# Kernel tuning notes

Hardware: AMD Instinct MI355X
Metric: run time of the kernel (lower is better)

Reference implementation:

```python
import jax, jax.numpy as jnp
import numpy as np
from jax import lax

DIM = 1024
HEADS = 16
HEAD_DIM = DIM // HEADS
BLOCK = 128          # block_size_q == block_size_kv
DECAY = 0.9          # decay_factor
SPIKE_TH = 0.5       # spike_threshold
K_WINNERS = 4        # k-winner-take-all along head_dim
HIDDEN = 4 * DIM     # SwiGLU hidden_mult=4.0
EPS = 1e-5


def _rmsnorm(x, w):
    norm = lax.rsqrt(jnp.mean(x * x, axis=-1, keepdims=True) + EPS)
    return w * x * norm


def _spike_kwta(k):
    # spiking threshold: pass activation only above SPIKE_TH
    k = jnp.where(k > SPIKE_TH, k, 0.0)
    # k-winners-take-all along head_dim
    thr = lax.top_k(k, K_WINNERS)[0][..., -1:]  # [B,T,H,1]
    return jnp.where(k >= thr, k, 0.0)


def _mix(h, Wr, Wk, Wv, Wo):
    # chunkwise (blockwise) decayed linear attention, RWKV-style
    B, T, _ = h.shape
    N = T // BLOCK
    r = jax.nn.sigmoid((h @ Wr).reshape(B, T, HEADS, HEAD_DIM))  # receptance
    k = _spike_kwta((h @ Wk).reshape(B, T, HEADS, HEAD_DIM))
    v = (h @ Wv).reshape(B, T, HEADS, HEAD_DIM)

    def chunks(a):  # [B,T,H,D] -> [N,B,L,H,D]
        return a.reshape(B, N, BLOCK, HEADS, HEAD_DIM).transpose(1, 0, 2, 3, 4)

    rc_all, kc_all, vc_all = chunks(r), chunks(k), chunks(v)

    t_idx = jnp.arange(BLOCK, dtype=h.dtype)
    w_in = (DECAY ** (t_idx + 1.0))[None, :, None, None]        # weight on incoming state
    w_out = (DECAY ** (BLOCK - 1.0 - t_idx))[None, :, None, None]  # weight into next state
    lm = t_idx[:, None] - t_idx[None, :]
    mask = jnp.where(lm >= 0, DECAY ** lm, 0.0)                 # [L,L] causal decay
    w_L = DECAY ** BLOCK

    def step(S, inp):
        rc, kc, vc = inp  # each [B,L,H,D]
        inter = jnp.einsum('blhd,bhde->blhe', rc * w_in, S)
        A = jnp.einsum('blhd,bmhd->bhlm', rc, kc) * mask
        intra = jnp.einsum('bhlm,bmhe->blhe', A, vc)
        S_new = w_L * S + jnp.einsum('blhd,blhe->bhde', kc * w_out, vc)
        return S_new, inter + intra

    S0 = jnp.zeros((B, HEADS, HEAD_DIM, HEAD_DIM), h.dtype)
    _, y = lax.scan(step, S0, (rc_all, kc_all, vc_all))  # y: [N,B,L,H,D]
    y = y.transpose(1, 0, 2, 3, 4).reshape(B, T, DIM)
    return y @ Wo


def setup_inputs() -> dict:
    key = jax.random.key(0)
    ks = jax.random.split(key, 9)
    s = 0.02
    return {
        'x': jax.random.normal(ks[0], (2, 1024, DIM), jnp.float32),
        'norm1_w': jnp.ones((DIM,), jnp.float32),
        'Wr': jax.random.normal(ks[1], (DIM, DIM), jnp.float32) * s,
        'Wk': jax.random.normal(ks[2], (DIM, DIM), jnp.float32) * s + 0.5,
        'Wv': jax.random.normal(ks[3], (DIM, DIM), jnp.float32) * s,
        'Wo': jax.random.normal(ks[4], (DIM, DIM), jnp.float32) * s,
        'norm2_w': jnp.ones((DIM,), jnp.float32),
        'w1': jax.random.normal(ks[5], (DIM, HIDDEN), jnp.float32) * s,
        'w2': jax.random.normal(ks[6], (DIM, HIDDEN), jnp.float32) * s,
        'w3': jax.random.normal(ks[7], (HIDDEN, DIM), jnp.float32) * s,
    }


def reference(x, norm1_w, Wr, Wk, Wv, Wo, norm2_w, w1, w2, w3):
    x = x + _mix(_rmsnorm(x, norm1_w), Wr, Wk, Wv, Wo)
    h = _rmsnorm(x, norm2_w)
    x = x + (jax.nn.silu(h @ w1) * (h @ w2)) @ w3
    return x
```

## Files before the change

### kernel.cpp

```cpp
#include <hip/hip_runtime.h>
#include <hip/hip_bf16.h>
#include <math.h>


#define DIMD 1024
#define BT   2048
#define HEADS 16
#define HD   64
#define CHUNK 128
#define NCHUNK 8
#define HIDDEN 4096
#define WL_128 1.3900845e-06f
#define LOG2D  (-0.15200309344504997f)

typedef __attribute__((ext_vector_type(4))) float f32x4;
typedef __attribute__((ext_vector_type(8))) short bf16x8;

__device__ __forceinline__ unsigned short f2bf(float f) {
    __hip_bfloat16 h = __float2bfloat16(f);
    return __builtin_bit_cast(unsigned short, h);
}
__device__ __forceinline__ float bf2f(unsigned short u) {
    __hip_bfloat16 h = __builtin_bit_cast(__hip_bfloat16, u);
    return __bfloat162float(h);
}
__device__ __forceinline__ void gload_lds16(const void* g, void* l) {
    __builtin_amdgcn_global_load_lds(
        (const __attribute__((address_space(1))) void*)g,
        (__attribute__((address_space(3))) void*)l,
        16, 0, 0);
}

__global__ __launch_bounds__(256) void prep_kernel(const float* __restrict__ x,
                                                   const float* __restrict__ norm1w,
                                                   const float* __restrict__ Wr,
                                                   const float* __restrict__ Wv,
                                                   const float* __restrict__ Wo,
                                                   const float* __restrict__ Wk,
                                                   const float* __restrict__ w1,
                                                   const float* __restrict__ w2,
                                                   const float* __restrict__ w3,
                                                   unsigned short* __restrict__ BtA,
                                                   unsigned short* __restrict__ wo_t,
                                                   unsigned short* __restrict__ wkB,
                                                   unsigned short* __restrict__ w1t,
                                                   unsigned short* __restrict__ w2t,
                                                   unsigned short* __restrict__ w3t,
                                                   unsigned short* __restrict__ hI) {
    __shared__ float t[64][65];
    __shared__ float red[4];
    int bid = blockIdx.x;
    if (bid < 4096) {
        const float* src; unsigned short* dst; int K, N, tile, mode = 0;
        if (bid < 256)       { src = Wr; dst = BtA;                 K = 1024; N = 1024; tile = bid; }
        else if (bid < 512)  { src = Wv; dst = BtA + 1024 * 1024;   K = 1024; N = 1024; tile = bid - 256; }
        else if (bid < 768)  { src = Wo; dst = wo_t;                K = 1024; N = 1024; tile = bid - 512; }
        else if (bid < 1024) { src = Wk; dst = wkB;                 K = 1024; N = 1024; tile = bid - 768; mode = 1; }
        else if (bid < 2048) { src = w1; dst = w1t; K = 1024; N = 4096; tile = bid - 1024; }
        else if (bid < 3072) { src = w2; dst = w2t; K = 1024; N = 4096; tile = bid - 2048; }
        else                 { src = w3; dst = w3t; K = 4096; N = 1024; tile = bid - 3072; }
        int xt = N >> 6;
        int bn = (tile % xt) << 6, bk = (tile / xt) << 6;
        int tx = threadIdx.x & 15, ty = threadIdx.x >> 4;
        #pragma unroll
// ... 37 lines not shown
        const float* xr = x + (size_t)row * DIMD;
        int i0 = threadIdx.x * 4;
        float4 v = *reinterpret_cast<const float4*>(xr + i0);
        float ss = v.x*v.x + v.y*v.y + v.z*v.z + v.w*v.w;
        #pragma unroll
        for (int off = 32; off; off >>= 1) ss += __shfl_xor(ss, off);
        if ((threadIdx.x & 63) == 0) red[threadIdx.x >> 6] = ss;
        __syncthreads();
        ss = red[0] + red[1] + red[2] + red[3];
        float norm = rsqrtf(ss * (1.0f / DIMD) + 1e-5f);
        float4 wv = *reinterpret_cast<const float4*>(norm1w + i0);
        float o[4];
        o[0] = wv.x * v.x * norm; o[1] = wv.y * v.y * norm;
        o[2] = wv.z * v.z * norm; o[3] = wv.w * v.w * norm;
        ushort4 u0, u1;
        unsigned short* q0 = (unsigned short*)&u0;
        unsigned short* q1 = (unsigned short*)&u1;
        #pragma unroll
        for (int j = 0; j < 4; ++j) {
            q0[j] = f2bf(o[j]);
            q1[j] = f2bf(o[j] - bf2f(q0[j]));
        }
        *reinterpret_cast<ushort4*>(hI + (size_t)row * 2048 + i0) = u0;
        *reinterpret_cast<ushort4*>(hI + (size_t)row * 2048 + 1024 + i0) = u1;
    }
}

__global__ __launch_bounds__(256) void proj_kernel(const unsigned short* __restrict__ hI,
                                                   const unsigned short* __restrict__ BtA,
                                                   const unsigned short* __restrict__ wkB,
                                                   unsigned short* __restrict__ r16,
                                                   unsigned short* __restrict__ v16,
                                                   unsigned short* __restrict__ k16) {
    __shared__ __align__(16) short As[128 * 64];
    __shared__ __align__(16) short Bs[128 * 64];
    const int tid = threadIdx.x;
    const int wv = tid >> 6, ln = tid & 63;
    const int g = ln >> 4, r = ln & 15;
    const int srow_off = ln >> 3;
    const int sslot = ln & 7;
    const short* Ag = (const short*)hI;

    if (blockIdx.x < 256) {
        const int bx = blockIdx.x & 15, by = blockIdx.x >> 4;
        const int bm = by << 7, bn = bx << 7;
        const int wr = (wv >> 1) << 6, wc = (wv & 1) << 6;
        const short* Bg = (const short*)BtA;
        f32x4 acc[4][4];
        #pragma unroll
        for (int i = 0; i < 4; ++i)
            #pragma unroll
            for (int j = 0; j < 4; ++j) acc[i][j] = (f32x4){0.f, 0.f, 0.f, 0.f};
        for (int k0 = 0; k0 < 1024; k0 += 64) {
            #pragma unroll
            for (int i = 0; i < 4; ++i) {
                int c = wv * 4 + i;
                int row = c * 8 + srow_off;
                int kcol = ((sslot ^ (row & 7)) << 3);
                gload_lds16(Ag + (size_t)(bm + row) * 2048 + k0 + kcol, &As[c * 512 + ln * 8]);
                gload_lds16(Bg + (size_t)(bn + row) * 1024 + k0 + kcol, &Bs[c * 512 + ln * 8]);
            }
            __syncthreads();
            #pragma unroll
            for (int kk = 0; kk < 2; ++kk) {
                bf16x8 af[4], bfr[4];
                #pragma unroll
                for (int mi = 0; mi < 4; ++mi) {
                    int row = wr + mi * 16 + r;
                    int slot = (kk * 4 + g) ^ (row & 7);
                    af[mi] = *reinterpret_cast<const bf16x8*>(&As[row * 64 + slot * 8]);
                }
                #pragma unroll
                for (int ni = 0; ni < 4; ++ni) {
                    int row = wc + ni * 16 + r;
                    int slot = (kk * 4 + g) ^ (row & 7);
                    bfr[ni] = *reinterpret_cast<const bf16x8*>(&Bs[row * 64 + slot * 8]);
                }
                #pragma unroll
                for (int mi = 0; mi < 4; ++mi)
                    #pragma unroll
                    for (int ni = 0; ni < 4; ++ni)
                        acc[mi][ni] = __builtin_amdgcn_mfma_f32_16x16x32_bf16(
                            af[mi], bfr[ni], acc[mi][ni], 0, 0, 0);
            }
            __syncthreads();
        }
        #pragma unroll
        for (int mi = 0; mi < 4; ++mi)
            #pragma unroll
            for (int q = 0; q < 4; ++q) {
                int row = bm + wr + mi * 16 + g * 4 + q;
                #pragma unroll
                for (int ni = 0; ni < 4; ++ni) {
                    int col = bn + wc + ni * 16 + r;
                    float vv = acc[mi][ni][q];
                    if (col < 1024) {
                        r16[(size_t)row * 1024 + col] = f2bf(1.0f / (1.0f + expf(-vv)));
                    } else {
                        v16[(size_t)row * 1024 + col - 1024] = f2bf(vv);
                    }
                }
            }
    } else {
        const int id = blockIdx.x - 256;
        const int bx = id & 7, by = id >> 3;
        const int bm = by << 6, bn = bx << 7;
        const int wr = (wv >> 1) << 5, wc = (wv & 1) << 6;
        const short* Bg = (const short*)wkB;
        f32x4 acc[2][4];
        #pragma unroll
        for (int i = 0; i < 2; ++i)
            #pragma unroll
            for (int j = 0; j < 4; ++j) acc[i][j] = (f32x4){0.f, 0.f, 0.f, 0.f};
        for (int k0 = 0; k0 < 3072; k0 += 64) {
            int srck0 = (k0 >= 1024) ? (k0 - 1024) : k0;
            #pragma unroll
            for (int i = 0; i < 2; ++i) {
                int c = wv * 2 + i;
                int row = c * 8 + srow_off;
                int kcol = ((sslot ^ (row & 7)) << 3);
                gload_lds16(Ag + (size_t)(bm + row) * 2048 + srck0 + kcol, &As[c * 512 + ln * 8]);
            }
            #pragma unroll
            for (int i = 0; i < 4; ++i) {
                int c = wv * 4 + i;
                int row = c * 8 + srow_off;
                int kcol = ((sslot ^ (row & 7)) << 3);
                gload_lds16(Bg + (size_t)(bn + row) * 3072 + k0 + kcol, &Bs[c * 512 + ln * 8]);
            }
            __syncthreads();
            #pragma unroll
            for (int kk = 0; kk < 2; ++kk) {
                bf16x8 af[2], bfr[4];
                #pragma unroll
                for (int mi = 0; mi < 2; ++mi) {
                    int row = wr + mi * 16 + r;
                    int slot = (kk * 4 + g) ^ (row & 7);
                    af[mi] = *reinterpret_cast<const bf16x8*>(&As[row * 64 + slot * 8]);
                }
                #pragma unroll
                for (int ni = 0; ni < 4; ++ni) {
                    int row = wc + ni * 16 + r;
                    int slot = (kk * 4 + g) ^ (row & 7);
                    bfr[ni] = *reinterpret_cast<const bf16x8*>(&Bs[row * 64 + slot * 8]);
                }
                #pragma unroll
                for (int mi = 0; mi < 2; ++mi)
                    #pragma unroll
                    for (int ni = 0; ni < 4; ++ni)
                        acc[mi][ni] = __builtin_amdgcn_mfma_f32_16x16x32_bf16(
                            af[mi], bfr[ni], acc[mi][ni], 0, 0, 0);
            }
            __syncthreads();
        }
        const unsigned long long gmask = 0xFFFFULL << (g * 16);
        #pragma unroll
        for (int mi = 0; mi < 2; ++mi) {
            #pragma unroll
            for (int q = 0; q < 4; ++q) {
                float s[4], cur4[4];
                #pragma unroll
                for (int ni = 0; ni < 4; ++ni) {
                    float a = acc[mi][ni][q];
                    s[ni] = (a > 0.5f) ? a : 0.0f;
                    cur4[ni] = s[ni];
                }
                float thr = 0.0f;
                #pragma unroll
                for (int it = 0; it < 4; ++it) {
                    float lm = fmaxf(fmaxf(cur4[0], cur4[1]), fmaxf(cur4[2], cur4[3]));
                    float gm = lm;
                    #pragma unroll
                    for (int off = 1; off < 16; off <<= 1) gm = fmaxf(gm, __shfl_xor(gm, off));
                    thr = gm;
                    unsigned long long ball = __ballot(lm == gm) & gmask;
                    int leader = __ffsll(ball) - 1;
                    if (ln == leader) {
                        bool done = false;
                        #pragma unroll
                        for (int ni = 0; ni < 4; ++ni) {
                            if (!done && cur4[ni] == gm) { cur4[ni] = -1.0f; done = true; }
                        }
                    }
                }
                int row = bm + wr + mi * 16 + g * 4 + q;
                #pragma unroll
                for (int ni = 0; ni < 4; ++ni) {
// ... 11 lines not shown
                                                       unsigned short* __restrict__ kwTg) {
    __shared__ float t[64][65];
    int z = blockIdx.z;
    const unsigned short* src = (z < 2) ? v16 : k16;
    unsigned short* dst = (z < 2) ? vTg : kwTg;
    int b = z & 1;
    int scaled = (z >= 2);
    int bc = blockIdx.x * 64, bt = blockIdx.y * 64;
    int tx = threadIdx.x & 15, ty = threadIdx.x >> 4;
    #pragma unroll
    for (int i = 0; i < 4; ++i) {
        ushort4 v = *reinterpret_cast<const ushort4*>(&src[(size_t)(b * 1024 + bt + ty + i * 16) * 1024 + bc + tx * 4]);
        t[ty + i * 16][tx * 4 + 0] = bf2f(v.x);
        t[ty + i * 16][tx * 4 + 1] = bf2f(v.y);
        t[ty + i * 16][tx * 4 + 2] = bf2f(v.z);
        t[ty + i * 16][tx * 4 + 3] = bf2f(v.w);
    }
    __syncthreads();
    #pragma unroll
    for (int i = 0; i < 4; ++i) {
        int crow = ty + i * 16;
        ushort4 o;
        unsigned short* po = (unsigned short*)&o;
        #pragma unroll
        for (int j = 0; j < 4; ++j) {
            int tl = bt + tx * 4 + j;
            float sc = scaled ? exp2f((float)(127 - (tl & 127)) * LOG2D) : 1.0f;
            po[j] = f2bf(t[tx * 4 + j][crow] * sc);
        }
        *reinterpret_cast<ushort4*>(&dst[(size_t)(b * 1024 + bc + crow) * 1024 + bt + tx * 4]) = o;
    }
}

template <int EPI, int MI>
__global__ __launch_bounds__(256) void gemm_bf16(const unsigned short* __restrict__ A,
                                                 const unsigned short* __restrict__ Bt,
                                                 void* __restrict__ Cout,
                                                 const float* __restrict__ add,
                                                 int M, int N, int K) {
    __shared__ __align__(16) short As[MI * 32 * 64];
    __shared__ __align__(16) short Bs[128 * 64];
    const int tid = threadIdx.x;
    const int wv = tid >> 6, ln = tid & 63;
    const int bm = blockIdx.y * (MI * 32), bn = blockIdx.x << 7;
    const int wr = (wv >> 1) * (MI * 16), wc = (wv & 1) << 6;
    const int g = ln >> 4, r16 = ln & 15;

    f32x4 acc[MI][4];
    #pragma unroll
    for (int i = 0; i < MI; ++i)
        #pragma unroll
        for (int j = 0; j < 4; ++j) acc[i][j] = (f32x4){0.f, 0.f, 0.f, 0.f};

    const short* Ag = (const short*)A;
    const short* Bg = (const short*)Bt;
    const int srow_off = ln >> 3;
    const int sslot = ln & 7;
    for (int k0 = 0; k0 < K; k0 += 64) {
        #pragma unroll
        for (int i = 0; i < MI; ++i) {
            int c = wv * MI + i;
            int row = c * 8 + srow_off;
            int kcol = ((sslot ^ (row & 7)) << 3);
            gload_lds16(Ag + (size_t)(bm + row) * K + k0 + kcol, &As[c * 512 + ln * 8]);
        }
        #pragma unroll
        for (int i = 0; i < 4; ++i) {
            int c = wv * 4 + i;
            int row = c * 8 + srow_off;
            int kcol = ((sslot ^ (row & 7)) << 3);
            gload_lds16(Bg + (size_t)(bn + row) * K + k0 + kcol, &Bs[c * 512 + ln * 8]);
        }
        __syncthreads();
        #pragma unroll
        for (int kk = 0; kk < 2; ++kk) {
            bf16x8 af[MI], bfr[4];
            #pragma unroll
            for (int mi = 0; mi < MI; ++mi) {
                int row = wr + mi * 16 + r16;
                int slot = (kk * 4 + g) ^ (row & 7);
                af[mi] = *reinterpret_cast<const bf16x8*>(&As[row * 64 + slot * 8]);
            }
            #pragma unroll
            for (int ni = 0; ni < 4; ++ni) {
                int row = wc + ni * 16 + r16;
                int slot = (kk * 4 + g) ^ (row & 7);
                bfr[ni] = *reinterpret_cast<const bf16x8*>(&Bs[row * 64 + slot * 8]);
            }
            #pragma unroll
            for (int mi = 0; mi < MI; ++mi)
                #pragma unroll
                for (int ni = 0; ni < 4; ++ni)
                    acc[mi][ni] = __builtin_amdgcn_mfma_f32_16x16x32_bf16(
                        af[mi], bfr[ni], acc[mi][ni], 0, 0, 0);
        }
        __syncthreads();
    }
    #pragma unroll
    for (int mi = 0; mi < MI; ++mi)
        #pragma unroll
        for (int q = 0; q < 4; ++q) {
            int row = bm + wr + mi * 16 + g * 4 + q;
            #pragma unroll
            for (int ni = 0; ni < 4; ++ni) {
                int col = bn + wc + ni * 16 + r16;
                float vv = acc[mi][ni][q];
                size_t o = (size_t)row * N + col;
                if (EPI == 2) vv += add[o];
                if (EPI == 3) ((unsigned short*)Cout)[o] = f2bf(vv);
                else          ((float*)Cout)[o] = vv;
            }
        }
}

__global__ __launch_bounds__(256) void gemm_splitk(const unsigned short* __restrict__ A,
                                                   const unsigned short* __restrict__ Bt,
                                                   float* __restrict__ P01,
                                                   float* __restrict__ P23,
                                                   int M, int N, int lda) {
    __shared__ __align__(16) short As[128 * 64];
    __shared__ __align__(16) short Bs[128 * 64];
    const int tid = threadIdx.x;
    const int wv = tid >> 6, ln = tid & 63;
    const int bm = blockIdx.y << 7, bn = blockIdx.x << 7;
    const int z = blockIdx.z;
    const int wr = (wv >> 1) << 6, wc = (wv & 1) << 6;
    const int g = ln >> 4, r16 = ln & 15;
    float* C = (z < 2) ? (P01 + (size_t)z * M * N) : (P23 + (size_t)(z - 2) * M * N);

    f32x4 acc[4][4];
    #pragma unroll
    for (int i = 0; i < 4; ++i)
        #pragma unroll
        for (int j = 0; j < 4; ++j) acc[i][j] = (f32x4){0.f, 0.f, 0.f, 0.f};

    const short* Ag = (const short*)A + z * 1024;
    const short* Bg = (const short*)Bt + z * 1024;
    const int srow_off = ln >> 3;
    const int sslot = ln & 7;
    for (int k0 = 0; k0 < 1024; k0 += 64) {
        #pragma unroll
        for (int i = 0; i < 4; ++i) {
            int c = wv * 4 + i;
            int row = c * 8 + srow_off;
            int kcol = ((sslot ^ (row & 7)) << 3);
            gload_lds16(Ag + (size_t)(bm + row) * lda + k0 + kcol, &As[c * 512 + ln * 8]);
            gload_lds16(Bg + (size_t)(bn + row) * lda + k0 + kcol, &Bs[c * 512 + ln * 8]);
        }
        __syncthreads();
        #pragma unroll
        for (int kk = 0; kk < 2; ++kk) {
            bf16x8 af[4], bfr[4];
            #pragma unroll
            for (int mi = 0; mi < 4; ++mi) {
                int row = wr + mi * 16 + r16;
                int slot = (kk * 4 + g) ^ (row & 7);
                af[mi] = *reinterpret_cast<const bf16x8*>(&As[row * 64 + slot * 8]);
            }
            #pragma unroll
            for (int ni = 0; ni < 4; ++ni) {
                int row = wc + ni * 16 + r16;
                int slot = (kk * 4 + g) ^ (row & 7);
                bfr[ni] = *reinterpret_cast<const bf16x8*>(&Bs[row * 64 + slot * 8]);
            }
            #pragma unroll
            for (int mi = 0; mi < 4; ++mi)
                #pragma unroll
                for (int ni = 0; ni < 4; ++ni)
                    acc[mi][ni] = __builtin_amdgcn_mfma_f32_16x16x32_bf16(
                        af[mi], bfr[ni], acc[mi][ni], 0, 0, 0);
        }
        __syncthreads();
    }
    #pragma unroll
    for (int mi = 0; mi < 4; ++mi)
        #pragma unroll
        for (int q = 0; q < 4; ++q) {
            int row = bm + wr + mi * 16 + g * 4 + q;
            #pragma unroll
            for (int ni = 0; ni < 4; ++ni)
                C[(size_t)row * N + bn + wc + ni * 16 + r16] = acc[mi][ni][q];
        }
}

__global__ __launch_bounds__(256) void reduce4_kernel(float* __restrict__ out,
                                                      const float* __restrict__ p0,
                                                      const float* __restrict__ p1,
                                                      const float* __restrict__ p2,
                                                      const float* __restrict__ p3) {
    size_t i = ((size_t)blockIdx.x * 256 + threadIdx.x) * 4;
    float4 o = *reinterpret_cast<float4*>(&out[i]);
    float4 a = *reinterpret_cast<const float4*>(&p0[i]);
    float4 b = *reinterpret_cast<const float4*>(&p1[i]);
    float4 c = *reinterpret_cast<const float4*>(&p2[i]);
    float4 d = *reinterpret_cast<const float4*>(&p3[i]);
    o.x += a.x + b.x + c.x + d.x;
    o.y += a.y + b.y + c.y + d.y;
    o.z += a.z + b.z + c.z + d.z;
    o.w += a.w + b.w + c.w + d.w;
    *reinterpret_cast<float4*>(&out[i]) = o;
}

__global__ __launch_bounds__(512) void gemm_swiglu_bf16(const unsigned short* __restrict__ A,
                                                        const unsigned short* __restrict__ B1t,
                                                        const unsigned short* __restrict__ B2t,
                                                        unsigned short* __restrict__ G,
                                                        int M, int N, int K) {
    __shared__ __align__(16) short SA[2][8192];
    __shared__ __align__(16) short SB1[2][8192];
    __shared__ __align__(16) short SB2[2][8192];
    const int tid = threadIdx.x;
    const int wv = tid >> 6, ln = tid & 63;
    const int bm = blockIdx.y << 7, bn = blockIdx.x << 7;
    const int wr = (wv >> 2) << 6, wc = (wv & 3) << 5;
    const int g = ln >> 4, r16 = ln & 15;
    const int srow = ln >> 3, sslot = ln & 7;

    f32x4 acc1[4][2], acc2[4][2];
    #pragma unroll
    for (int i = 0; i < 4; ++i)
        #pragma unroll
        for (int j = 0; j < 2; ++j) {
            acc1[i][j] = (f32x4){0.f, 0.f, 0.f, 0.f};
            acc2[i][j] = (f32x4){0.f, 0.f, 0.f, 0.f};
        }

    const short* Ag  = (const short*)A + (size_t)bm * K;
    const short* B1g = (const short*)B1t + (size_t)bn * K;
    const short* B2g = (const short*)B2t + (size_t)bn * K;

    #define SW_STAGE(k0, b)                                                        \
        {                                                                          \
            _Pragma("unroll")                                                      \
            for (int i = 0; i < 2; ++i) {                                          \
                int c = wv * 2 + i;                                                \
                int row = c * 8 + srow;                                            \
                int kc = ((sslot ^ (row & 7)) << 3);                               \
                gload_lds16(Ag  + (size_t)row * K + (k0) + kc, &SA[b][c * 512 + ln * 8]);  \
                gload_lds16(B1g + (size_t)row * K + (k0) + kc, &SB1[b][c * 512 + ln * 8]); \
                gload_lds16(B2g + (size_t)row * K + (k0) + kc, &SB2[b][c * 512 + ln * 8]); \
            }                                                                      \
        }

    const int NT = K >> 6;
    SW_STAGE(0, 0);
    asm volatile("s_waitcnt vmcnt(0)" ::: "memory");
    __builtin_amdgcn_s_barrier();
    asm volatile("" ::: "memory");
    for (int t = 0; t < NT; ++t) {
        int cur = t & 1;
        if (t + 1 < NT) SW_STAGE((t + 1) << 6, cur ^ 1);
        asm volatile("s_waitcnt vmcnt(6)" ::: "memory");
        __builtin_amdgcn_s_barrier();
        asm volatile("" ::: "memory");
        #pragma unroll
        for (int kk = 0; kk < 2; ++kk) {
            bf16x8 af[4], b1f[2], b2f[2];
            #pragma unroll
            for (int mi = 0; mi < 4; ++mi) {
                int row = wr + mi * 16 + r16;
                int slot = (kk * 4 + g) ^ (row & 7);
                af[mi] = *reinterpret_cast<const bf16x8*>(&SA[cur][row * 64 + slot * 8]);
            }
            #pragma unroll
            for (int ni = 0; ni < 2; ++ni) {
                int row = wc + ni * 16 + r16;
                int slot = (kk * 4 + g) ^ (row & 7);
                b1f[ni] = *reinterpret_cast<const bf16x8*>(&SB1[cur][row * 64 + slot * 8]);
                b2f[ni] = *reinterpret_cast<const bf16x8*>(&SB2[cur][row * 64 + slot * 8]);
            }
            #pragma unroll
            for (int mi = 0; mi < 4; ++mi)
                #pragma unroll
                for (int ni = 0; ni < 2; ++ni) {
                    acc1[mi][ni] = __builtin_amdgcn_mfma_f32_16x16x32_bf16(
                        af[mi], b1f[ni], acc1[mi][ni], 0, 0, 0);
                    acc2[mi][ni] = __builtin_amdgcn_mfma_f32_16x16x32_bf16(
                        af[mi], b2f[ni], acc2[mi][ni], 0, 0, 0);
                }
        }
        asm volatile("" ::: "memory");
        __builtin_amdgcn_s_barrier();
        asm volatile("" ::: "memory");
    }
    #undef SW_STAGE
    #pragma unroll
    for (int mi = 0; mi < 4; ++mi)
        #pragma unroll
        for (int q = 0; q < 4; ++q) {
            int row = bm + wr + mi * 16 + g * 4 + q;
            #pragma unroll
            for (int ni = 0; ni < 2; ++ni) {
                int col = bn + wc + ni * 16 + r16;
                float a = acc1[mi][ni][q];
                float vv = a / (1.0f + expf(-a)) * acc2[mi][ni][q];
                G[(size_t)row * N + col] = f2bf(vv);
            }
        }
}

__global__ __launch_bounds__(256) void rms2_kernel(const float* __restrict__ x,
                                                   const float* __restrict__ w,
                                                   unsigned short* __restrict__ h) {
    int row = blockIdx.x;
    const float* xr = x + (size_t)row * DIMD;
    int i0 = threadIdx.x * 4;
    float4 v = *reinterpret_cast<const float4*>(xr + i0);
    float ss = v.x*v.x + v.y*v.y + v.z*v.z + v.w*v.w;
    #pragma unroll
    for (int off = 32; off; off >>= 1) ss += __shfl_xor(ss, off);
    __shared__ float red[4];
    if ((threadIdx.x & 63) == 0) red[threadIdx.x >> 6] = ss;
    __syncthreads();
    ss = red[0] + red[1] + red[2] + red[3];
    float norm = rsqrtf(ss * (1.0f / DIMD) + 1e-5f);
    float4 wv = *reinterpret_cast<const float4*>(w + i0);
// ... 238 lines not shown
    char* ws = (char*)d_ws;
    (void)in_sizes; (void)n_in; (void)out_size; (void)ws_size;

    const size_t MB = 1048576;
    unsigned short* BtA  = (unsigned short*)(ws + 0 * MB);
    unsigned short* wkB  = (unsigned short*)(ws + 4 * MB);
    unsigned short* wo_t = (unsigned short*)(ws + 10 * MB);
    unsigned short* w1t  = (unsigned short*)(ws + 12 * MB);
    unsigned short* w2t  = (unsigned short*)(ws + 20 * MB);
    unsigned short* w3t  = (unsigned short*)(ws + 28 * MB);
    unsigned short* hI   = (unsigned short*)(ws + 36 * MB);
    unsigned short* r16  = (unsigned short*)(ws + 44 * MB);
    unsigned short* v16  = (unsigned short*)(ws + 48 * MB);
    unsigned short* k16  = (unsigned short*)(ws + 52 * MB);
    unsigned short* vTg  = (unsigned short*)(ws + 56 * MB);
    unsigned short* kwTg = (unsigned short*)(ws + 60 * MB);
    float*          Cbuf = (float*)(ws + 64 * MB);
    unsigned short* STg  = (unsigned short*)(ws + 68 * MB);
    unsigned short* y16  = (unsigned short*)(ws + 70 * MB);
    unsigned short* h0b  = (unsigned short*)(ws + 36 * MB);
    unsigned short* g16  = (unsigned short*)(ws + 56 * MB);
    float*          p01  = (float*)(ws + 12 * MB);
    float*          p23  = (float*)(ws + 40 * MB);

    dim3 blk(256);

    prep_kernel<<<6144, blk, 0, stream>>>(x, norm1w, Wr, Wv, Wo, Wk, w1, w2, w3,
                                          BtA, wo_t, wkB, w1t, w2t, w3t, hI);
    proj_kernel<<<512, blk, 0, stream>>>(hI, BtA, wkB, r16, v16, k16);
    transpose_attn4<<<dim3(16, 16, 4), blk, 0, stream>>>(v16, k16, vTg, kwTg);
    attn_state_mfma<<<NCHUNK * 32, blk, 0, stream>>>(vTg, kwTg, Cbuf);
    attn_scan_kernel<<<32, blk, 0, stream>>>(Cbuf, STg);
    attn_out_mfma<<<NCHUNK * 32, blk, 0, stream>>>(r16, k16, vTg, STg, y16);
    gemm_bf16<2, 2><<<dim3(8, 32), blk, 0, stream>>>(y16, wo_t, out, x, BT, DIMD, DIMD);
    rms2_kernel<<<BT, blk, 0, stream>>>(out, norm2w, h0b);
    gemm_swiglu_bf16<<<dim3(32, 16), dim3(512), 0, stream>>>(h0b, w1t, w2t, g16, BT, HIDDEN, DIMD);
    gemm_splitk<<<dim3(8, 16, 4), blk, 0, stream>>>(g16, w3t, p01, p23, BT, DIMD, HIDDEN);
    reduce4_kernel<<<2048, blk, 0, stream>>>(out, p01, p01 + (size_t)BT * DIMD,
                                             p23, p23 + (size_t)BT * DIMD);
}
```

Measured before the change: 201.1 us.

## Double-buffer LDS loads in projection, Wo and split-K GEMMs; triple-buffer SwiGLU

Converts the projection, output-projection and split-K GEMM main loops from single-buffered load/sync/compute into double-buffered pipelines. The next K-tile's global-to-LDS loads are issued before computing the current one, with explicit vmcnt waits and raw barriers in place of __syncthreads. The SwiGLU GEMM goes from two to three stages so loads run two tiles ahead. The aim is to hide global memory latency behind MFMA work, at the cost of doubling or tripling LDS use per block, which may lower occupancy, especially the roughly 144KB triple buffer in the SwiGLU kernel.

```diff
diff --git a/kernel.cpp b/kernel.cpp
--- a/kernel.cpp
+++ b/kernel.cpp
@@ -30,6 +30,8 @@
         (__attribute__((address_space(3))) void*)l,
         16, 0, 0);
 }
+#define VMCNT(n) asm volatile("s_waitcnt vmcnt(" #n ")" ::: "memory")
+#define BAR()    do { __builtin_amdgcn_s_barrier(); asm volatile("" ::: "memory"); } while (0)
 
 __global__ __launch_bounds__(256) void prep_kernel(const float* __restrict__ x,
                                                    const float* __restrict__ norm1w,
@@ -133,35 +135,39 @@
                                                    unsigned short* __restrict__ r16,
                                                    unsigned short* __restrict__ v16,
                                                    unsigned short* __restrict__ k16) {
-    __shared__ __align__(16) short As[128 * 64];
-    __shared__ __align__(16) short Bs[128 * 64];
+    __shared__ __align__(16) short SA[2][8192];
+    __shared__ __align__(16) short SB[2][8192];
     const int tid = threadIdx.x;
     const int wv = tid >> 6, ln = tid & 63;
     const int g = ln >> 4, r = ln & 15;
-    const int srow_off = ln >> 3;
-    const int sslot = ln & 7;
-    const short* Ag = (const short*)hI;
+    const int srow = ln >> 3, sslot = ln & 7;
 
     if (blockIdx.x < 256) {
         const int bx = blockIdx.x & 15, by = blockIdx.x >> 4;
         const int bm = by << 7, bn = bx << 7;
         const int wr = (wv >> 1) << 6, wc = (wv & 1) << 6;
-        const short* Bg = (const short*)BtA;
+        const short* Ag = (const short*)hI + (size_t)bm * 2048;
+        const short* Bg = (const short*)BtA + (size_t)bn * 1024;
         f32x4 acc[4][4];
         #pragma unroll
         for (int i = 0; i < 4; ++i)
             #pragma unroll
             for (int j = 0; j < 4; ++j) acc[i][j] = (f32x4){0.f, 0.f, 0.f, 0.f};
-        for (int k0 = 0; k0 < 1024; k0 += 64) {
-            #pragma unroll
-            for (int i = 0; i < 4; ++i) {
-                int c = wv * 4 + i;
-                int row = c * 8 + srow_off;
-                int kcol = ((sslot ^ (row & 7)) << 3);
-                gload_lds16(Ag + (size_t)(bm + row) * 2048 + k0 + kcol, &As[c * 512 + ln * 8]);
-                gload_lds16(Bg + (size_t)(bn + row) * 1024 + k0 + kcol, &Bs[c * 512 + ln * 8]);
-            }
-            __syncthreads();
+        #define PA_STAGE(k0, b)                                                            \
+            { _Pragma("unroll")                                                            \
+              for (int i = 0; i < 4; ++i) {                                                \
+                  int c = wv * 4 + i;                                                      \
+                  int row = c * 8 + srow;                                                  \
+                  int kc = ((sslot ^ (row & 7)) << 3);                                     \
+                  gload_lds16(Ag + (size_t)row * 2048 + (k0) + kc, &SA[b][c * 512 + ln * 8]); \
+                  gload_lds16(Bg + (size_t)row * 1024 + (k0) + kc, &SB[b][c * 512 + ln * 8]); \
+              } }
+        PA_STAGE(0, 0);
+        for (int t = 0; t < 16; ++t) {
+            int cur = t & 1;
+            if (t + 1 < 16) { PA_STAGE((t + 1) << 6, cur ^ 1); VMCNT(8); }
+            else            { VMCNT(0); }
+            BAR();
             #pragma unroll
             for (int kk = 0; kk < 2; ++kk) {
                 bf16x8 af[4], bfr[4];
@@ -169,13 +175,13 @@
                 for (int mi = 0; mi < 4; ++mi) {
                     int row = wr + mi * 16 + r;
                     int slot = (kk * 4 + g) ^ (row & 7);
-                    af[mi] = *reinterpret_cast<const bf16x8*>(&As[row * 64 + slot * 8]);
+                    af[mi] = *reinterpret_cast<const bf16x8*>(&SA[cur][row * 64 + slot * 8]);
                 }
                 #pragma unroll
                 for (int ni = 0; ni < 4; ++ni) {
                     int row = wc + ni * 16 + r;
                     int slot = (kk * 4 + g) ^ (row & 7);
-                    bfr[ni] = *reinterpret_cast<const bf16x8*>(&Bs[row * 64 + slot * 8]);
+                    bfr[ni] = *reinterpret_cast<const bf16x8*>(&SB[cur][row * 64 + slot * 8]);
                 }
                 #pragma unroll
                 for (int mi = 0; mi < 4; ++mi)
@@ -184,8 +190,9 @@
                         acc[mi][ni] = __builtin_amdgcn_mfma_f32_16x16x32_bf16(
                             af[mi], bfr[ni], acc[mi][ni], 0, 0, 0);
             }
-            __syncthreads();
-        }
+            BAR();
+        }
+        #undef PA_STAGE
         #pragma unroll
         for (int mi = 0; mi < 4; ++mi)
             #pragma unroll
@@ -207,29 +214,37 @@
         const int bx = id & 7, by = id >> 3;
         const int bm = by << 6, bn = bx << 7;
         const int wr = (wv >> 1) << 5, wc = (wv & 1) << 6;
-        const short* Bg = (const short*)wkB;
+        const short* Ag = (const short*)hI + (size_t)bm * 2048;
+        const short* Bg = (const short*)wkB + (size_t)bn * 3072;
         f32x4 acc[2][4];
         #pragma unroll
         for (int i = 0; i < 2; ++i)
             #pragma unroll
             for (int j = 0; j < 4; ++j) acc[i][j] = (f32x4){0.f, 0.f, 0.f, 0.f};
-        for (int k0 = 0; k0 < 3072; k0 += 64) {
-            int srck0 = (k0 >= 1024) ? (k0 - 1024) : k0;
-            #pragma unroll
-            for (int i = 0; i < 2; ++i) {
-                int c = wv * 2 + i;
-                int row = c * 8 + srow_off;
-                int kcol = ((sslot ^ (row & 7)) << 3);
-                gload_lds16(Ag + (size_t)(bm + row) * 2048 + srck0 + kcol, &As[c * 512 + ln * 8]);
-            }
-            #pragma unroll
-            for (int i = 0; i < 4; ++i) {
-                int c = wv * 4 + i;
-                int row = c * 8 + srow_off;
-                int kcol = ((sslot ^ (row & 7)) << 3);
-                gload_lds16(Bg + (size_t)(bn + row) * 3072 + k0 + kcol, &Bs[c * 512 + ln * 8]);
-            }
-            __syncthreads();
+        #define PB_STAGE(k0, b)                                                            \
+            { int srck0 = ((k0) >= 1024 && (k0) < 2048) ? ((k0) - 1024) : (((k0) >= 2048) ? ((k0) - 2048) : (k0)); \
+              (void)srck0;                                                                 \
+              int ak0 = ((k0) >= 1024) ? ((k0) - 1024) : (k0);                             \
+              _Pragma("unroll")                                                            \
+              for (int i = 0; i < 2; ++i) {                                                \
+                  int c = wv * 2 + i;                                                      \
+                  int row = c * 8 + srow;                                                  \
+                  int kc = ((sslot ^ (row & 7)) << 3);                                     \
+                  gload_lds16(Ag + (size_t)row * 2048 + ak0 + kc, &SA[b][c * 512 + ln * 8]); \
+              }                                                                            \
+              _Pragma("unroll")                                                            \
+              for (int i = 0; i < 4; ++i) {                                                \
+                  int c = wv * 4 + i;                                                      \
+                  int row = c * 8 + srow;                                                  \
+                  int kc = ((sslot ^ (row & 7)) << 3);                                     \
+                  gload_lds16(Bg + (size_t)row * 3072 + (k0) + kc, &SB[b][c * 512 + ln * 8]); \
+              } }
+        PB_STAGE(0, 0);
+        for (int t = 0; t < 48; ++t) {
+            int cur = t & 1;
+            if (t + 1 < 48) { PB_STAGE((t + 1) << 6, cur ^ 1); VMCNT(6); }
+            else            { VMCNT(0); }
+            BAR();
             #pragma unroll
             for (int kk = 0; kk < 2; ++kk) {
                 bf16x8 af[2], bfr[4];
@@ -237,13 +252,13 @@
                 for (int mi = 0; mi < 2; ++mi) {
                     int row = wr + mi * 16 + r;
                     int slot = (kk * 4 + g) ^ (row & 7);
-                    af[mi] = *reinterpret_cast<const bf16x8*>(&As[row * 64 + slot * 8]);
+                    af[mi] = *reinterpret_cast<const bf16x8*>(&SA[cur][row * 64 + slot * 8]);
                 }
                 #pragma unroll
                 for (int ni = 0; ni < 4; ++ni) {
                     int row = wc + ni * 16 + r;
                     int slot = (kk * 4 + g) ^ (row & 7);
-                    bfr[ni] = *reinterpret_cast<const bf16x8*>(&Bs[row * 64 + slot * 8]);
+                    bfr[ni] = *reinterpret_cast<const bf16x8*>(&SB[cur][row * 64 + slot * 8]);
                 }
                 #pragma unroll
                 for (int mi = 0; mi < 2; ++mi)
@@ -252,8 +267,9 @@
                         acc[mi][ni] = __builtin_amdgcn_mfma_f32_16x16x32_bf16(
                             af[mi], bfr[ni], acc[mi][ni], 0, 0, 0);
             }
-            __syncthreads();
-        }
+            BAR();
+        }
+        #undef PB_STAGE
         const unsigned long long gmask = 0xFFFFULL << (g * 16);
         #pragma unroll
         for (int mi = 0; mi < 2; ++mi) {
@@ -331,83 +347,85 @@
     }
 }
 
-template <int EPI, int MI>
-__global__ __launch_bounds__(256) void gemm_bf16(const unsigned short* __restrict__ A,
-                                                 const unsigned short* __restrict__ Bt,
-                                                 void* __restrict__ Cout,
-                                                 const float* __restrict__ add,
-                                                 int M, int N, int K) {
-    __shared__ __align__(16) short As[MI * 32 * 64];
-    __shared__ __align__(16) short Bs[128 * 64];
+__global__ __launch_bounds__(256) void gemm_wo(const unsigned short* __restrict__ A,
+                                               const unsigned short* __restrict__ Bt,
+                                               float* __restrict__ Cout,
+                                               const float* __restrict__ add,
+                                               int M, int N, int K) {
+    __shared__ __align__(16) short SA[2][4096];
+    __shared__ __align__(16) short SB[2][8192];
     const int tid = threadIdx.x;
     const int wv = tid >> 6, ln = tid & 63;
-    const int bm = blockIdx.y * (MI * 32), bn = blockIdx.x << 7;
-    const int wr = (wv >> 1) * (MI * 16), wc = (wv & 1) << 6;
+    const int bm = blockIdx.y << 6, bn = blockIdx.x << 7;
+    const int wr = (wv >> 1) << 5, wc = (wv & 1) << 6;
     const int g = ln >> 4, r16 = ln & 15;
-
-    f32x4 acc[MI][4];
-    #pragma unroll
-    for (int i = 0; i < MI; ++i)
+    const int srow = ln >> 3, sslot = ln & 7;
+
+    f32x4 acc[2][4];
+    #pragma unroll
+    for (int i = 0; i < 2; ++i)
         #pragma unroll
         for (int j = 0; j < 4; ++j) acc[i][j] = (f32x4){0.f, 0.f, 0.f, 0.f};
 
-    const short* Ag = (const short*)A;
-    const short* Bg = (const short*)Bt;
-    const int srow_off = ln >> 3;
-    const int sslot = ln & 7;
-    for (int k0 = 0; k0 < K; k0 += 64) {
-        #pragma unroll
-        for (int i = 0; i < MI; ++i) {
-            int c = wv * MI + i;
-            int row = c * 8 + srow_off;
-            int kcol = ((sslot ^ (row & 7)) << 3);
-            gload_lds16(Ag + (size_t)(bm + row) * K + k0 + kcol, &As[c * 512 + ln * 8]);
-        }
-        #pragma unroll
-        for (int i = 0; i < 4; ++i) {
-            int c = wv * 4 + i;
-            int row = c * 8 + srow_off;
-            int kcol = ((sslot ^ (row & 7)) << 3);
-            gload_lds16(Bg + (size_t)(bn + row) * K + k0 + kcol, &Bs[c * 512 + ln * 8]);
-        }
-        __syncthreads();
+    const short* Ag = (const short*)A + (size_t)bm * K;
+    const short* Bg = (const short*)Bt + (size_t)bn * K;
+    #define WO_STAGE(k0, b)                                                            \
+        { _Pragma("unroll")                                                            \
+          for (int i = 0; i < 2; ++i) {                                                \
+              int c = wv * 2 + i;                                                      \
+              int row = c * 8 + srow;                                                  \
+              int kc = ((sslot ^ (row & 7)) << 3);                                     \
+              gload_lds16(Ag + (size_t)row * K + (k0) + kc, &SA[b][c * 512 + ln * 8]); \
+          }                                                                            \
+          _Pragma("unroll")                                                            \
+          for (int i = 0; i < 4; ++i) {                                                \
+              int c = wv * 4 + i;                                                      \
+              int row = c * 8 + srow;                                                  \
+              int kc = ((sslot ^ (row & 7)) << 3);                                     \
+              gload_lds16(Bg + (size_t)row * K + (k0) + kc, &SB[b][c * 512 + ln * 8]); \
+          } }
+    const int NT = K >> 6;
+    WO_STAGE(0, 0);
+    for (int t = 0; t < NT; ++t) {
+        int cur = t & 1;
+        if (t + 1 < NT) { WO_STAGE((t + 1) << 6, cur ^ 1); VMCNT(6); }
+        else            { VMCNT(0); }
+        BAR();
         #pragma unroll
         for (int kk = 0; kk < 2; ++kk) {
-            bf16x8 af[MI], bfr[4];
-            #pragma unroll
-            for (int mi = 0; mi < MI; ++mi) {
+            bf16x8 af[2], bfr[4];
+            #pragma unroll
+            for (int mi = 0; mi < 2; ++mi) {
                 int row = wr + mi * 16 + r16;
                 int slot = (kk * 4 + g) ^ (row & 7);
-                af[mi] = *reinterpret_cast<const bf16x8*>(&As[row * 64 + slot * 8]);
+                af[mi] = *reinterpret_cast<const bf16x8*>(&SA[cur][row * 64 + slot * 8]);
             }
             #pragma unroll
             for (int ni = 0; ni < 4; ++ni) {
                 int row = wc + ni * 16 + r16;
                 int slot = (kk * 4 + g) ^ (row & 7);
-                bfr[ni] = *reinterpret_cast<const bf16x8*>(&Bs[row * 64 + slot * 8]);
-            }
-            #pragma unroll
-            for (int mi = 0; mi < MI; ++mi)
+                bfr[ni] = *reinterpret_cast<const bf16x8*>(&SB[cur][row * 64 + slot * 8]);
+            }
+            #pragma unroll
+            for (int mi = 0; mi < 2; ++mi)
                 #pragma unroll
                 for (int ni = 0; ni < 4; ++ni)
                     acc[mi][ni] = __builtin_amdgcn_mfma_f32_16x16x32_bf16(
                         af[mi], bfr[ni], acc[mi][ni], 0, 0, 0);
         }
-        __syncthreads();
-    }
-    #pragma unroll
-    for (int mi = 0; mi < MI; ++mi)
+        BAR();
+    }
+    #undef WO_STAGE
+    #pragma unroll
+    for (int mi = 0; mi < 2; ++mi)
         #pragma unroll
         for (int q = 0; q < 4; ++q) {
             int row = bm + wr + mi * 16 + g * 4 + q;
             #pragma unroll
             for (int ni = 0; ni < 4; ++ni) {
                 int col = bn + wc + ni * 16 + r16;
-                float vv = acc[mi][ni][q];
                 size_t o = (size_t)row * N + col;
-                if (EPI == 2) vv += add[o];
-                if (EPI == 3) ((unsigned short*)Cout)[o] = f2bf(vv);
-                else          ((float*)Cout)[o] = vv;
+                Cout[o] = acc[mi][ni][q] + add[o];
             }
         }
 }
@@ -417,14 +435,15 @@
                                                    float* __restrict__ P01,
                                                    float* __restrict__ P23,
                                                    int M, int N, int lda) {
-    __shared__ __align__(16) short As[128 * 64];
-    __shared__ __align__(16) short Bs[128 * 64];
+    __shared__ __align__(16) short SA[2][8192];
+    __shared__ __align__(16) short SB[2][8192];
     const int tid = threadIdx.x;
     const int wv = tid >> 6, ln = tid & 63;
     const int bm = blockIdx.y << 7, bn = blockIdx.x << 7;
     const int z = blockIdx.z;
     const int wr = (wv >> 1) << 6, wc = (wv & 1) << 6;
     const int g = ln >> 4, r16 = ln & 15;
+    const int srow = ln >> 3, sslot = ln & 7;
     float* C = (z < 2) ? (P01 + (size_t)z * M * N) : (P23 + (size_t)(z - 2) * M * N);
 
     f32x4 acc[4][4];
@@ -433,20 +452,23 @@
         #pragma unroll
         for (int j = 0; j < 4; ++j) acc[i][j] = (f32x4){0.f, 0.f, 0.f, 0.f};
 
-    const short* Ag = (const short*)A + z * 1024;
-    const short* Bg = (const short*)Bt + z * 1024;
-    const int srow_off = ln >> 3;
-    const int sslot = ln & 7;
-    for (int k0 = 0; k0 < 1024; k0 += 64) {
-        #pragma unroll
-        for (int i = 0; i < 4; ++i) {
-            int c = wv * 4 + i;
-            int row = c * 8 + srow_off;
-            int kcol = ((sslot ^ (row & 7)) << 3);
-            gload_lds16(Ag + (size_t)(bm + row) * lda + k0 + kcol, &As[c * 512 + ln * 8]);
-            gload_lds16(Bg + (size_t)(bn + row) * lda + k0 + kcol, &Bs[c * 512 + ln * 8]);
-        }
-        __syncthreads();
+    const short* Ag = (const short*)A + (size_t)bm * lda + z * 1024;
+    const short* Bg = (const short*)Bt + (size_t)bn * lda + z * 1024;
+    #define SK_STAGE(k0, b)                                                              \
+        { _Pragma("unroll")                                                              \
+          for (int i = 0; i < 4; ++i) {                                                  \
+              int c = wv * 4 + i;                                                        \
+              int row = c * 8 + srow;                                                    \
+              int kc = ((sslot ^ (row & 7)) << 3);                                       \
+              gload_lds16(Ag + (size_t)row * lda + (k0) + kc, &SA[b][c * 512 + ln * 8]); \
+              gload_lds16(Bg + (size_t)row * lda + (k0) + kc, &SB[b][c * 512 + ln * 8]); \
+          } }
+    SK_STAGE(0, 0);
+    for (int t = 0; t < 16; ++t) {
+        int cur = t & 1;
+        if (t + 1 < 16) { SK_STAGE((t + 1) << 6, cur ^ 1); VMCNT(8); }
+        else            { VMCNT(0); }
+        BAR();
         #pragma unroll
         for (int kk = 0; kk < 2; ++kk) {
             bf16x8 af[4], bfr[4];
@@ -454,13 +476,13 @@
             for (int mi = 0; mi < 4; ++mi) {
                 int row = wr + mi * 16 + r16;
                 int slot = (kk * 4 + g) ^ (row & 7);
-                af[mi] = *reinterpret_cast<const bf16x8*>(&As[row * 64 + slot * 8]);
+                af[mi] = *reinterpret_cast<const bf16x8*>(&SA[cur][row * 64 + slot * 8]);
             }
             #pragma unroll
             for (int ni = 0; ni < 4; ++ni) {
                 int row = wc + ni * 16 + r16;
                 int slot = (kk * 4 + g) ^ (row & 7);
-                bfr[ni] = *reinterpret_cast<const bf16x8*>(&Bs[row * 64 + slot * 8]);
+                bfr[ni] = *reinterpret_cast<const bf16x8*>(&SB[cur][row * 64 + slot * 8]);
             }
             #pragma unroll
             for (int mi = 0; mi < 4; ++mi)
@@ -469,8 +491,9 @@
                     acc[mi][ni] = __builtin_amdgcn_mfma_f32_16x16x32_bf16(
                         af[mi], bfr[ni], acc[mi][ni], 0, 0, 0);
         }
-        __syncthreads();
-    }
+        BAR();
+    }
+    #undef SK_STAGE
     #pragma unroll
     for (int mi = 0; mi < 4; ++mi)
         #pragma unroll
@@ -505,9 +528,9 @@
                                                         const unsigned short* __restrict__ B2t,
                                                         unsigned short* __restrict__ G,
                                                         int M, int N, int K) {
-    __shared__ __align__(16) short SA[2][8192];
-    __shared__ __align__(16) short SB1[2][8192];
-    __shared__ __align__(16) short SB2[2][8192];
+    __shared__ __align__(16) short SA[3][8192];
+    __shared__ __align__(16) short SB1[3][8192];
+    __shared__ __align__(16) short SB2[3][8192];
     const int tid = threadIdx.x;
     const int wv = tid >> 6, ln = tid & 63;
     const int bm = blockIdx.y << 7, bn = blockIdx.x << 7;
@@ -529,29 +552,25 @@
     const short* B2g = (const short*)B2t + (size_t)bn * K;
 
     #define SW_STAGE(k0, b)                                                        \
-        {                                                                          \
-            _Pragma("unroll")                                                      \
-            for (int i = 0; i < 2; ++i) {                                          \
-                int c = wv * 2 + i;                                                \
-                int row = c * 8 + srow;                                            \
-                int kc = ((sslot ^ (row & 7)) << 3);                               \
-                gload_lds16(Ag  + (size_t)row * K + (k0) + kc, &SA[b][c * 512 + ln * 8]);  \
-                gload_lds16(B1g + (size_t)row * K + (k0) + kc, &SB1[b][c * 512 + ln * 8]); \
-                gload_lds16(B2g + (size_t)row * K + (k0) + kc, &SB2[b][c * 512 + ln * 8]); \
-            }                                                                      \
-        }
+        { _Pragma("unroll")                                                        \
+          for (int i = 0; i < 2; ++i) {                                            \
+              int c = wv * 2 + i;                                                  \
+              int row = c * 8 + srow;                                              \
+              int kc = ((sslot ^ (row & 7)) << 3);                                 \
+              gload_lds16(Ag  + (size_t)row * K + (k0) + kc, &SA[b][c * 512 + ln * 8]);  \
+              gload_lds16(B1g + (size_t)row * K + (k0) + kc, &SB1[b][c * 512 + ln * 8]); \
+              gload_lds16(B2g + (size_t)row * K + (k0) + kc, &SB2[b][c * 512 + ln * 8]); \
+          } }
 
     const int NT = K >> 6;
     SW_STAGE(0, 0);
-    asm volatile("s_waitcnt vmcnt(0)" ::: "memory");
-    __builtin_amdgcn_s_barrier();
-    asm volatile("" ::: "memory");
+    SW_STAGE(64, 1);
     for (int t = 0; t < NT; ++t) {
-        int cur = t & 1;
-        if (t + 1 < NT) SW_STAGE((t + 1) << 6, cur ^ 1);
-        asm volatile("s_waitcnt vmcnt(6)" ::: "memory");
-        __builtin_amdgcn_s_barrier();
-        asm volatile("" ::: "memory");
+        int cur = t % 3;
+        if (t + 2 < NT)      { SW_STAGE((t + 2) << 6, (t + 2) % 3); VMCNT(12); }
+        else if (t + 1 < NT) { VMCNT(6); }
+        else                 { VMCNT(0); }
+        BAR();
         #pragma unroll
         for (int kk = 0; kk < 2; ++kk) {
             bf16x8 af[4], b1f[2], b2f[2];
@@ -578,9 +597,7 @@
                         af[mi], b2f[ni], acc2[mi][ni], 0, 0, 0);
                 }
         }
-        asm volatile("" ::: "memory");
-        __builtin_amdgcn_s_barrier();
-        asm volatile("" ::: "memory");
+        BAR();
     }
     #undef SW_STAGE
     #pragma unroll
@@ -885,7 +902,7 @@
     attn_state_mfma<<<NCHUNK * 32, blk, 0, stream>>>(vTg, kwTg, Cbuf);
     attn_scan_kernel<<<32, blk, 0, stream>>>(Cbuf, STg);
     attn_out_mfma<<<NCHUNK * 32, blk, 0, stream>>>(r16, k16, vTg, STg, y16);
-    gemm_bf16<2, 2><<<dim3(8, 32), blk, 0, stream>>>(y16, wo_t, out, x, BT, DIMD, DIMD);
+    gemm_wo<<<dim3(8, 32), blk, 0, stream>>>(y16, wo_t, out, x, BT, DIMD, DIMD);
     rms2_kernel<<<BT, blk, 0, stream>>>(out, norm2w, h0b);
     gemm_swiglu_bf16<<<dim3(32, 16), dim3(512), 0, stream>>>(h0b, w1t, w2t, g16, BT, HIDDEN, DIMD);
     gemm_splitk<<<dim3(8, 16, 4), blk, 0, stream>>>(g16, w3t, p01, p23, BT, DIMD, HIDDEN);
```

Measured after the change: 202.1 us. About the same (+0.5%).

## Double-buffer the Wo GEMM and triple-buffer the SwiGLU GEMM prefetch

Applied to the files above, without the earlier changes.

The Wo projection GEMM changes from a single-buffered loop with __syncthreads into a double-buffered loop. It prefetches the next K tile through global_load_lds while the current tile runs on MFMA, with explicit vmcnt waits. The SwiGLU GEMM goes from two to three LDS stages and prefetches two tiles ahead. Both changes aim to hide global memory latency behind compute. The cost is more LDS per block: the SwiGLU kernel grows to about 144KB, which may cut occupancy or exceed the per-CU LDS limit.

```diff
diff --git a/kernel.cpp b/kernel.cpp
--- a/kernel.cpp
+++ b/kernel.cpp
@@ -30,6 +30,8 @@
         (__attribute__((address_space(3))) void*)l,
         16, 0, 0);
 }
+#define VMCNT(n) asm volatile("s_waitcnt vmcnt(" #n ")" ::: "memory")
+#define BAR()    do { __builtin_amdgcn_s_barrier(); asm volatile("" ::: "memory"); } while (0)
 
 __global__ __launch_bounds__(256) void prep_kernel(const float* __restrict__ x,
                                                    const float* __restrict__ norm1w,
@@ -214,13 +216,13 @@
             #pragma unroll
             for (int j = 0; j < 4; ++j) acc[i][j] = (f32x4){0.f, 0.f, 0.f, 0.f};
         for (int k0 = 0; k0 < 3072; k0 += 64) {
-            int srck0 = (k0 >= 1024) ? (k0 - 1024) : k0;
+            int ak0 = (k0 >= 1024) ? (k0 - 1024) : k0;
             #pragma unroll
             for (int i = 0; i < 2; ++i) {
                 int c = wv * 2 + i;
                 int row = c * 8 + srow_off;
                 int kcol = ((sslot ^ (row & 7)) << 3);
-                gload_lds16(Ag + (size_t)(bm + row) * 2048 + srck0 + kcol, &As[c * 512 + ln * 8]);
+                gload_lds16(Ag + (size_t)(bm + row) * 2048 + ak0 + kcol, &As[c * 512 + ln * 8]);
             }
             #pragma unroll
             for (int i = 0; i < 4; ++i) {
@@ -331,83 +333,85 @@
     }
 }
 
-template <int EPI, int MI>
-__global__ __launch_bounds__(256) void gemm_bf16(const unsigned short* __restrict__ A,
-                                                 const unsigned short* __restrict__ Bt,
-                                                 void* __restrict__ Cout,
-                                                 const float* __restrict__ add,
-                                                 int M, int N, int K) {
-    __shared__ __align__(16) short As[MI * 32 * 64];
-    __shared__ __align__(16) short Bs[128 * 64];
+__global__ __launch_bounds__(256) void gemm_wo(const unsigned short* __restrict__ A,
+                                               const unsigned short* __restrict__ Bt,
+                                               float* __restrict__ Cout,
+                                               const float* __restrict__ add,
+                                               int M, int N, int K) {
+    __shared__ __align__(16) short SA[2][4096];
+    __shared__ __align__(16) short SB[2][8192];
     const int tid = threadIdx.x;
     const int wv = tid >> 6, ln = tid & 63;
-    const int bm = blockIdx.y * (MI * 32), bn = blockIdx.x << 7;
-    const int wr = (wv >> 1) * (MI * 16), wc = (wv & 1) << 6;
+    const int bm = blockIdx.y << 6, bn = blockIdx.x << 7;
+    const int wr = (wv >> 1) << 5, wc = (wv & 1) << 6;
     const int g = ln >> 4, r16 = ln & 15;
-
-    f32x4 acc[MI][4];
-    #pragma unroll
-    for (int i = 0; i < MI; ++i)
+    const int srow = ln >> 3, sslot = ln & 7;
+
+    f32x4 acc[2][4];
+    #pragma unroll
+    for (int i = 0; i < 2; ++i)
         #pragma unroll
         for (int j = 0; j < 4; ++j) acc[i][j] = (f32x4){0.f, 0.f, 0.f, 0.f};
 
-    const short* Ag = (const short*)A;
-    const short* Bg = (const short*)Bt;
-    const int srow_off = ln >> 3;
-    const int sslot = ln & 7;
-    for (int k0 = 0; k0 < K; k0 += 64) {
-        #pragma unroll
-        for (int i = 0; i < MI; ++i) {
-            int c = wv * MI + i;
-            int row = c * 8 + srow_off;
-            int kcol = ((sslot ^ (row & 7)) << 3);
-            gload_lds16(Ag + (size_t)(bm + row) * K + k0 + kcol, &As[c * 512 + ln * 8]);
-        }
-        #pragma unroll
-        for (int i = 0; i < 4; ++i) {
-            int c = wv * 4 + i;
-            int row = c * 8 + srow_off;
-            int kcol = ((sslot ^ (row & 7)) << 3);
-            gload_lds16(Bg + (size_t)(bn + row) * K + k0 + kcol, &Bs[c * 512 + ln * 8]);
-        }
-        __syncthreads();
+    const short* Ag = (const short*)A + (size_t)bm * K;
+    const short* Bg = (const short*)Bt + (size_t)bn * K;
+    #define WO_STAGE(k0, b)                                                            \
+        { _Pragma("unroll")                                                            \
+          for (int i = 0; i < 2; ++i) {                                                \
+              int c = wv * 2 + i;                                                      \
+              int row = c * 8 + srow;                                                  \
+              int kc = ((sslot ^ (row & 7)) << 3);                                     \
+              gload_lds16(Ag + (size_t)row * K + (k0) + kc, &SA[b][c * 512 + ln * 8]); \
+          }                                                                            \
+          _Pragma("unroll")                                                            \
+          for (int i = 0; i < 4; ++i) {                                                \
+              int c = wv * 4 + i;                                                      \
+              int row = c * 8 + srow;                                                  \
+              int kc = ((sslot ^ (row & 7)) << 3);                                     \
+              gload_lds16(Bg + (size_t)row * K + (k0) + kc, &SB[b][c * 512 + ln * 8]); \
+          } }
+    const int NT = K >> 6;
+    WO_STAGE(0, 0);
+    for (int t = 0; t < NT; ++t) {
+        int cur = t & 1;
+        if (t + 1 < NT) { WO_STAGE((t + 1) << 6, cur ^ 1); VMCNT(6); }
+        else            { VMCNT(0); }
+        BAR();
         #pragma unroll
         for (int kk = 0; kk < 2; ++kk) {
-            bf16x8 af[MI], bfr[4];
-            #pragma unroll
-            for (int mi = 0; mi < MI; ++mi) {
+            bf16x8 af[2], bfr[4];
+            #pragma unroll
+            for (int mi = 0; mi < 2; ++mi) {
                 int row = wr + mi * 16 + r16;
                 int slot = (kk * 4 + g) ^ (row & 7);
-                af[mi] = *reinterpret_cast<const bf16x8*>(&As[row * 64 + slot * 8]);
+                af[mi] = *reinterpret_cast<const bf16x8*>(&SA[cur][row * 64 + slot * 8]);
             }
             #pragma unroll
             for (int ni = 0; ni < 4; ++ni) {
                 int row = wc + ni * 16 + r16;
                 int slot = (kk * 4 + g) ^ (row & 7);
-                bfr[ni] = *reinterpret_cast<const bf16x8*>(&Bs[row * 64 + slot * 8]);
-            }
-            #pragma unroll
-            for (int mi = 0; mi < MI; ++mi)
+                bfr[ni] = *reinterpret_cast<const bf16x8*>(&SB[cur][row * 64 + slot * 8]);
+            }
+            #pragma unroll
+            for (int mi = 0; mi < 2; ++mi)
                 #pragma unroll
                 for (int ni = 0; ni < 4; ++ni)
                     acc[mi][ni] = __builtin_amdgcn_mfma_f32_16x16x32_bf16(
                         af[mi], bfr[ni], acc[mi][ni], 0, 0, 0);
         }
-        __syncthreads();
-    }
-    #pragma unroll
-    for (int mi = 0; mi < MI; ++mi)
+        BAR();
+    }
+    #undef WO_STAGE
+    #pragma unroll
+    for (int mi = 0; mi < 2; ++mi)
         #pragma unroll
         for (int q = 0; q < 4; ++q) {
             int row = bm + wr + mi * 16 + g * 4 + q;
             #pragma unroll
             for (int ni = 0; ni < 4; ++ni) {
                 int col = bn + wc + ni * 16 + r16;
-                float vv = acc[mi][ni][q];
                 size_t o = (size_t)row * N + col;
-                if (EPI == 2) vv += add[o];
-                if (EPI == 3) ((unsigned short*)Cout)[o] = f2bf(vv);
-                else          ((float*)Cout)[o] = vv;
+                Cout[o] = acc[mi][ni][q] + add[o];
             }
         }
 }
@@ -425,6 +429,8 @@
     const int z = blockIdx.z;
     const int wr = (wv >> 1) << 6, wc = (wv & 1) << 6;
     const int g = ln >> 4, r16 = ln & 15;
+    const int srow_off = ln >> 3;
+    const int sslot = ln & 7;
     float* C = (z < 2) ? (P01 + (size_t)z * M * N) : (P23 + (size_t)(z - 2) * M * N);
 
     f32x4 acc[4][4];
@@ -435,8 +441,6 @@
 
     const short* Ag = (const short*)A + z * 1024;
     const short* Bg = (const short*)Bt + z * 1024;
-    const int srow_off = ln >> 3;
-    const int sslot = ln & 7;
     for (int k0 = 0; k0 < 1024; k0 += 64) {
         #pragma unroll
         for (int i = 0; i < 4; ++i) {
@@ -505,9 +509,9 @@
                                                         const unsigned short* __restrict__ B2t,
                                                         unsigned short* __restrict__ G,
                                                         int M, int N, int K) {
-    __shared__ __align__(16) short SA[2][8192];
-    __shared__ __align__(16) short SB1[2][8192];
-    __shared__ __align__(16) short SB2[2][8192];
+    __shared__ __align__(16) short SA[3][8192];
+    __shared__ __align__(16) short SB1[3][8192];
+    __shared__ __align__(16) short SB2[3][8192];
     const int tid = threadIdx.x;
     const int wv = tid >> 6, ln = tid & 63;
     const int bm = blockIdx.y << 7, bn = blockIdx.x << 7;
@@ -529,29 +533,25 @@
     const short* B2g = (const short*)B2t + (size_t)bn * K;
 
     #define SW_STAGE(k0, b)                                                        \
-        {                                                                          \
-            _Pragma("unroll")                                                      \
-            for (int i = 0; i < 2; ++i) {                                          \
-                int c = wv * 2 + i;                                                \
-                int row = c * 8 + srow;                                            \
-                int kc = ((sslot ^ (row & 7)) << 3);                               \
-                gload_lds16(Ag  + (size_t)row * K + (k0) + kc, &SA[b][c * 512 + ln * 8]);  \
-                gload_lds16(B1g + (size_t)row * K + (k0) + kc, &SB1[b][c * 512 + ln * 8]); \
-                gload_lds16(B2g + (size_t)row * K + (k0) + kc, &SB2[b][c * 512 + ln * 8]); \
-            }                                                                      \
-        }
+        { _Pragma("unroll")                                                        \
+          for (int i = 0; i < 2; ++i) {                                            \
+              int c = wv * 2 + i;                                                  \
+              int row = c * 8 + srow;                                              \
+              int kc = ((sslot ^ (row & 7)) << 3);                                 \
+              gload_lds16(Ag  + (size_t)row * K + (k0) + kc, &SA[b][c * 512 + ln * 8]);  \
+              gload_lds16(B1g + (size_t)row * K + (k0) + kc, &SB1[b][c * 512 + ln * 8]); \
+              gload_lds16(B2g + (size_t)row * K + (k0) + kc, &SB2[b][c * 512 + ln * 8]); \
+          } }
 
     const int NT = K >> 6;
     SW_STAGE(0, 0);
-    asm volatile("s_waitcnt vmcnt(0)" ::: "memory");
-    __builtin_amdgcn_s_barrier();
-    asm volatile("" ::: "memory");
+    SW_STAGE(64, 1);
     for (int t = 0; t < NT; ++t) {
-        int cur = t & 1;
-        if (t + 1 < NT) SW_STAGE((t + 1) << 6, cur ^ 1);
-        asm volatile("s_waitcnt vmcnt(6)" ::: "memory");
-        __builtin_amdgcn_s_barrier();
-        asm volatile("" ::: "memory");
+        int cur = t % 3;
+        if (t + 2 < NT)      { SW_STAGE((t + 2) << 6, (t + 2) % 3); VMCNT(12); }
+        else if (t + 1 < NT) { VMCNT(6); }
+        else                 { VMCNT(0); }
+        BAR();
         #pragma unroll
         for (int kk = 0; kk < 2; ++kk) {
             bf16x8 af[4], b1f[2], b2f[2];
@@ -578,9 +578,7 @@
                         af[mi], b2f[ni], acc2[mi][ni], 0, 0, 0);
                 }
         }
-        asm volatile("" ::: "memory");
-        __builtin_amdgcn_s_barrier();
-        asm volatile("" ::: "memory");
+        BAR();
     }
     #undef SW_STAGE
     #pragma unroll
@@ -885,7 +883,7 @@
     attn_state_mfma<<<NCHUNK * 32, blk, 0, stream>>>(vTg, kwTg, Cbuf);
     attn_scan_kernel<<<32, blk, 0, stream>>>(Cbuf, STg);
     attn_out_mfma<<<NCHUNK * 32, blk, 0, stream>>>(r16, k16, vTg, STg, y16);
-    gemm_bf16<2, 2><<<dim3(8, 32), blk, 0, stream>>>(y16, wo_t, out, x, BT, DIMD, DIMD);
+    gemm_wo<<<dim3(8, 32), blk, 0, stream>>>(y16, wo_t, out, x, BT, DIMD, DIMD);
     rms2_kernel<<<BT, blk, 0, stream>>>(out, norm2w, h0b);
     gemm_swiglu_bf16<<<dim3(32, 16), dim3(512), 0, stream>>>(h0b, w1t, w2t, g16, BT, HIDDEN, DIMD);
     gemm_splitk<<<dim3(8, 16, 4), blk, 0, stream>>>(g16, w3t, p01, p23, BT, DIMD, HIDDEN);
```

After: 199.5 us. About the same (-0.8%).
